# Optimization experiments

Measured on AMD Instinct MI355X. Metric: run time of the kernel, lower is better.

## Reference

```python
import jax, jax.numpy as jnp
import numpy as np
from math import ceil

CAPACITY_FACTOR = 2.0
MIN_CAPACITY = 4


def setup_inputs() -> dict:
    key = jax.random.key(0)
    ks = jax.random.split(key, 4)
    B, S, D, Di, E = 4, 2048, 1024, 4096, 8
    x = jax.random.normal(ks[0], (B, S, D), dtype=jnp.float32)
    Wr = jax.random.normal(ks[1], (D, E), dtype=jnp.float32) * (D ** -0.5)
    W1 = jax.random.normal(ks[2], (E, D, Di), dtype=jnp.float32) * (D ** -0.5)
    b1 = jnp.zeros((E, Di), dtype=jnp.float32)
    W2 = jax.random.normal(ks[3], (E, Di, D), dtype=jnp.float32) * (Di ** -0.5)
    b2 = jnp.zeros((E, D), dtype=jnp.float32)
    return {"x": x, "Wr": Wr, "W1": W1, "b1": b1, "W2": W2, "b2": b2}


def reference(x, Wr, W1, b1, W2, b2):
    B, S, D = x.shape
    E = Wr.shape[1]
    N = B * S
    k = max(MIN_CAPACITY, ceil(N * CAPACITY_FACTOR / E))  # expert capacity (static)

    xt = x.reshape(N, D)
    scores = jax.nn.softmax(xt @ Wr, axis=-1)          # [N, E] router probs
    G, idx = jax.lax.top_k(scores.T, k)                 # [E, k]: each expert picks top-k tokens

    # dispatch: equivalent to P @ x with P = one_hot(idx, N)
    X_in = xt[idx]                                      # [E, k, D]

    # per-expert MLP (batched over experts): Linear -> GELU(exact) -> Linear
    h = jax.nn.gelu(jnp.einsum('ekd,edh->ekh', X_in, W1) + b1[:, None, :], approximate=False)
    X_e = jnp.einsum('ekh,ehd->ekd', h, W2) + b2[:, None, :]  # [E, k, D]

    # combine: einsum('ijl,ij,ijd->ld', P, G, X_e) == scatter-add of G*X_e at idx
    contrib = (G[..., None] * X_e).reshape(E * k, D)
    out = jnp.zeros((N, D), dtype=x.dtype).at[idx.reshape(-1)].add(contrib)
    return out.reshape(B, S, D)
```

## Files before the change

### kernel.cpp

```cpp
#include <hip/hip_runtime.h>
#include <hip/hip_bf16.h>
#include <cstdint>
#include <cstddef>

#define NTOK 8192
#define DMODEL 1024
#define DFF 4096
#define NEXP 8
#define CAP 2048

typedef __attribute__((ext_vector_type(8))) __bf16 bf16x8;
typedef __attribute__((ext_vector_type(4))) float f32x4;

__device__ __forceinline__ void gload16(const void* g, void* l) {
  __builtin_amdgcn_global_load_lds(
      (__attribute__((address_space(1))) void*)(g),
      (__attribute__((address_space(3))) void*)(l),
      16, 0, 0);
}
#define VMWAIT_(n) asm volatile("s_waitcnt vmcnt(" #n ")" ::: "memory")
#define VMWAIT(n) VMWAIT_(n)
#define MEMFENCE asm volatile("" ::: "memory")

__global__ __launch_bounds__(256) void zero_f32(float* p, int n4) {
  int i = blockIdx.x * blockDim.x + threadIdx.x;
  int stride = gridDim.x * blockDim.x;
  float4 z = make_float4(0.f, 0.f, 0.f, 0.f);
  for (; i < n4; i += stride) ((float4*)p)[i] = z;
}

__global__ __launch_bounds__(256) void router_kernel(
    const float* __restrict__ x, const float* __restrict__ Wr,
    float* __restrict__ scoresT, __hip_bfloat16* __restrict__ xb) {
  const int lane = threadIdx.x & 63;
  const int t = blockIdx.x * 4 + (threadIdx.x >> 6);
  const float* xr = x + (size_t)t * DMODEL;
  float acc[NEXP];
#pragma unroll
  for (int j = 0; j < NEXP; ++j) acc[j] = 0.f;
#pragma unroll
  for (int it = 0; it < DMODEL / 64; ++it) {
    int d = it * 64 + lane;
    float xv = xr[d];
    xb[(size_t)t * DMODEL + d] = __float2bfloat16(xv);
    const float4* w = (const float4*)(Wr + (size_t)d * NEXP);
    float4 w0 = w[0], w1 = w[1];
    acc[0] += xv * w0.x; acc[1] += xv * w0.y; acc[2] += xv * w0.z; acc[3] += xv * w0.w;
    acc[4] += xv * w1.x; acc[5] += xv * w1.y; acc[6] += xv * w1.z; acc[7] += xv * w1.w;
  }
#pragma unroll
  for (int off = 32; off; off >>= 1) {
#pragma unroll
    for (int j = 0; j < NEXP; ++j) acc[j] += __shfl_xor(acc[j], off);
  }
  float m = acc[0];
#pragma unroll
  for (int j = 1; j < NEXP; ++j) m = fmaxf(m, acc[j]);
  float s = 0.f;
#pragma unroll
  for (int j = 0; j < NEXP; ++j) { acc[j] = expf(acc[j] - m); s += acc[j]; }
  float inv = 1.f / s;
  if (lane < NEXP) scoresT[(size_t)lane * NTOK + t] = acc[lane] * inv;
}

__global__ __launch_bounds__(256) void topk_kernel(
    const float* __restrict__ scoresT, float* __restrict__ G, int* __restrict__ IDX) {
  __shared__ uint32_t sb[NTOK];
  __shared__ uint32_t hist[256];
  __shared__ uint32_t s_prefix, s_rem;
  __shared__ uint32_t eq_list[256];
  __shared__ uint32_t eq_cnt, gt_cnt;
  const int e = blockIdx.x, tid = threadIdx.x;
  const float* se = scoresT + (size_t)e * NTOK;
  for (int i = tid; i < NTOK; i += 256) sb[i] = __float_as_uint(se[i]);
  if (tid == 0) { s_prefix = 0u; s_rem = CAP; eq_cnt = 0u; gt_cnt = 0u; }
  __syncthreads();
  for (int r = 0; r < 4; ++r) {
    const int shift = 24 - 8 * r;
    for (int i = tid; i < 256; i += 256) hist[i] = 0u;
    __syncthreads();
    uint32_t pfx = s_prefix;
    for (int i = tid; i < NTOK; i += 256) {
      uint32_t b = sb[i];
      if (((b >> shift) >> 8) == pfx) atomicAdd(&hist[(b >> shift) & 255u], 1u);
    }
    __syncthreads();
    if (tid == 0) {
      uint32_t rem = s_rem, cum = 0u;
      int d = 255;
      for (; d > 0; --d) {
        if (cum + hist[d] >= rem) break;
        cum += hist[d];
      }
      s_prefix = (pfx << 8) | (uint32_t)d;
      s_rem = rem - cum;
    }
    __syncthreads();
  }
  const uint32_t T = s_prefix, need = s_rem;
  for (int i = tid; i < NTOK; i += 256) {
    uint32_t b = sb[i];
    if (b > T) {
      uint32_t p = atomicAdd(&gt_cnt, 1u);
      IDX[(size_t)e * CAP + p] = i;
      G[(size_t)e * CAP + p] = __uint_as_float(b);
    } else if (b == T) {
      uint32_t c = atomicAdd(&eq_cnt, 1u);
      if (c < 256u) eq_list[c] = (uint32_t)i;
    }
  }
  __syncthreads();
  if (tid == 0) {
    uint32_t base = gt_cnt;
    uint32_t c = eq_cnt < 256u ? eq_cnt : 256u;
    for (uint32_t s = 0; s < need; ++s) {
      uint32_t mv = 0xFFFFFFFFu; int mi = 0;
      for (uint32_t j = 0; j < c; ++j)
        if (eq_list[j] < mv) { mv = eq_list[j]; mi = (int)j; }
      eq_list[mi] = 0xFFFFFFFFu;
      IDX[(size_t)e * CAP + base + s] = (int)mv;
      G[(size_t)e * CAP + base + s] = __uint_as_float(T);
    }
  }
}

__global__ __launch_bounds__(256) void transpose_cvt(
    const float* __restrict__ in, __hip_bfloat16* __restrict__ out, int R, int C) {
  __shared__ float tile[32][33];
  const int e = blockIdx.z;
  const float* ine = in + (size_t)e * R * C;
  __hip_bfloat16* oute = out + (size_t)e * R * C;
  const int c0 = blockIdx.x * 32, r0 = blockIdx.y * 32;
  const int tx = threadIdx.x, ty = threadIdx.y;
#pragma unroll
  for (int i = 0; i < 4; ++i)
    tile[ty + i * 8][tx] = ine[(size_t)(r0 + ty + i * 8) * C + (c0 + tx)];
  __syncthreads();
#pragma unroll
  for (int i = 0; i < 4; ++i)
    oute[(size_t)(c0 + ty + i * 8) * R + (r0 + tx)] =
        __float2bfloat16(tile[tx][ty + i * 8]);
}


template <int NKT>
__device__ __forceinline__ void gemm_core_v5(
    const char* pa0, const char* pa1, const char* pa2, const char* pa3,
    const char* pb0, const char* pb1, const char* pb2, const char* pb3,
    char* smem, f32x4 (&acc)[8][4]) {
  const int tid = threadIdx.x;
  const int wave = tid >> 6, lane = tid & 63;
  const int wm = wave >> 2, wn = wave & 3;
  const int lrow = lane & 15, lgrp = lane >> 4;
  const int dst = tid * 16;

  const char* pa[4] = {pa0, pa1, pa2, pa3};
  const char* pb[4] = {pb0, pb1, pb2, pb3};

  int offA[8][2], offB[4][2];
#pragma unroll
  for (int mi = 0; mi < 8; ++mi) {
    int rL = wm * 128 + mi * 16 + lrow;
#pragma unroll
    for (int ks = 0; ks < 2; ++ks)
      offA[mi][ks] = rL * 128 + (((ks * 4 + lgrp) + rL & 7) << 4);
  }
#pragma unroll
  for (int mi = 0; mi < 8; ++mi)
#pragma unroll
    for (int ks = 0; ks < 2; ++ks) {
      int rL = wm * 128 + mi * 16 + lrow;
      offA[mi][ks] = rL * 128 + ((((ks * 4 + lgrp) + rL) & 7) << 4);
    }
#pragma unroll
  for (int ni = 0; ni < 4; ++ni) {
    int rL = wn * 64 + ni * 16 + lrow;
#pragma unroll
    for (int ks = 0; ks < 2; ++ks)
      offB[ni][ks] = 32768 + rL * 128 + ((((ks * 4 + lgrp) + rL) & 7) << 4);
  }

#pragma unroll
  for (int g = 0; g < 4; ++g) { gload16(pa[g], smem + g * 8192 + dst); pa[g] += 128; }
#pragma unroll
  for (int g = 0; g < 4; ++g) { gload16(pb[g], smem + 32768 + g * 8192 + dst); pb[g] += 128; }
#pragma unroll
  for (int g = 0; g < 4; ++g) { gload16(pa[g], smem + 65536 + g * 8192 + dst); pa[g] += 128; }
#pragma unroll
  for (int g = 0; g < 4; ++g) { gload16(pb[g], smem + 65536 + 32768 + g * 8192 + dst); pb[g] += 128; }

  for (int kt = 0; kt < NKT; ++kt) {
    char* buf = smem + ((kt & 1) << 16);
    if (kt < NKT - 1) { VMWAIT(8); } else { VMWAIT(0); }
    __builtin_amdgcn_s_barrier();
    MEMFENCE;

    bf16x8 av[8], bv[4];
#pragma unroll
    for (int mi = 0; mi < 8; ++mi) av[mi] = *(const bf16x8*)(buf + offA[mi][0]);
#pragma unroll
    for (int ni = 0; ni < 4; ++ni) bv[ni] = *(const bf16x8*)(buf + offB[ni][0]);

    __builtin_amdgcn_s_setprio(1);
#pragma unroll
    for (int mi = 0; mi < 8; ++mi)
#pragma unroll
      for (int ni = 0; ni < 4; ++ni)
        acc[mi][ni] = __builtin_amdgcn_mfma_f32_16x16x32_bf16(
            av[mi], bv[ni], acc[mi][ni], 0, 0, 0);
    __builtin_amdgcn_s_setprio(0);

    bf16x8 av2[8], bv2[4];
#pragma unroll
    for (int mi = 0; mi < 8; ++mi) av2[mi] = *(const bf16x8*)(buf + offA[mi][1]);
#pragma unroll
    for (int ni = 0; ni < 4; ++ni) bv2[ni] = *(const bf16x8*)(buf + offB[ni][1]);

    asm volatile("s_waitcnt lgkmcnt(0)" ::: "memory");
    __builtin_amdgcn_s_barrier();
    MEMFENCE;
    if (kt < NKT - 2) {
#pragma unroll
      for (int g = 0; g < 4; ++g) { gload16(pa[g], buf + g * 8192 + dst); pa[g] += 128; }
#pragma unroll
      for (int g = 0; g < 4; ++g) { gload16(pb[g], buf + 32768 + g * 8192 + dst); pb[g] += 128; }
    }
    __builtin_amdgcn_sched_barrier(0);
    __builtin_amdgcn_s_setprio(1);
#pragma unroll
    for (int mi = 0; mi < 8; ++mi)
#pragma unroll
      for (int ni = 0; ni < 4; ++ni)
        acc[mi][ni] = __builtin_amdgcn_mfma_f32_16x16x32_bf16(
            av2[mi], bv2[ni], acc[mi][ni], 0, 0, 0);
    __builtin_amdgcn_s_setprio(0);
  }
}

__device__ __forceinline__ float gelu_tanh(float v) {
  float t = 0.7978845608028654f * (v + 0.044715f * v * v * v);
  float e = __expf(2.f * t);
  float th = 1.f - 2.f / (e + 1.f);
  return 0.5f * v * (1.f + th);
}

__global__ __launch_bounds__(512, 2) void gemm1_kernel(
    const __hip_bfloat16* __restrict__ xb,
    const __hip_bfloat16* __restrict__ W1t,
    const float* __restrict__ b1,
    const int* __restrict__ IDX,
    __hip_bfloat16* __restrict__ h, int e0, int nblk) {
  __shared__ __align__(16) char smem[131072];
  int lin = blockIdx.x;
  { int q = nblk >> 3; lin = (lin & 7) * q + (lin >> 3); }
  const int tm = lin & 7, tn = (lin >> 3) & 15, ez = lin >> 7;
  const int e = e0 + ez;
  const int tid = threadIdx.x, wave = tid >> 6, lane = tid & 63;
  const int wm = wave >> 2, wn = wave & 3;
  const int lrow = lane & 15, lgrp = lane >> 4;

  const int r0 = tid >> 3;
  const int ksrc = (((tid & 7) - r0) & 7) * 16;
  const char* pa[4]; const char* pb[4];
#pragma unroll
  for (int g = 0; g < 4; ++g) {
    int m = g * 64 + r0;
    int tok = IDX[e * CAP + tm * 256 + m];
    pa[g] = (const char*)(xb + (size_t)tok * DMODEL) + ksrc;
    int n = g * 64 + r0;
    pb[g] = (const char*)(W1t + ((size_t)e * DFF + tn * 256 + n) * DMODEL) + ksrc;
  }

  f32x4 acc[8][4];
  f32x4 zero = {0.f, 0.f, 0.f, 0.f};
#pragma unroll
  for (int mi = 0; mi < 8; ++mi)
#pragma unroll
    for (int ni = 0; ni < 4; ++ni) acc[mi][ni] = zero;

  gemm_core_v5<DMODEL / 64>(pa[0], pa[1], pa[2], pa[3],
                            pb[0], pb[1], pb[2], pb[3], smem, acc);

  __hip_bfloat16* he = h + (size_t)ez * CAP * DFF;
  const float* b1e = b1 + (size_t)e * DFF;
  float bvals[4];
#pragma unroll
  for (int ni = 0; ni < 4; ++ni)
    bvals[ni] = b1e[tn * 256 + wn * 64 + ni * 16 + lrow];
#pragma unroll
  for (int mi = 0; mi < 8; ++mi) {
#pragma unroll
    for (int j = 0; j < 4; ++j) {
      int row = tm * 256 + wm * 128 + mi * 16 + lgrp * 4 + j;
      __hip_bfloat16* hrow = he + (size_t)row * DFF;
#pragma unroll
      for (int ni = 0; ni < 4; ++ni) {
        int col = tn * 256 + wn * 64 + ni * 16 + lrow;
        float v = acc[mi][ni][j] + bvals[ni];
        hrow[col] = __float2bfloat16(gelu_tanh(v));
      }
    }
  }
}

__global__ __launch_bounds__(512, 2) void gemm2_kernel(
    const __hip_bfloat16* __restrict__ h,
    const __hip_bfloat16* __restrict__ W2t,
    const float* __restrict__ b2,
    const int* __restrict__ IDX, const float* __restrict__ G,
    float* __restrict__ out, int e0, int nblk) {
  __shared__ __align__(16) char smem[131072];
  int lin = blockIdx.x;
  { int q = nblk >> 3; lin = (lin & 7) * q + (lin >> 3); }
  const int tm = lin & 7, tn = (lin >> 3) & 3, ez = lin >> 5;
  const int e = e0 + ez;
  const int tid = threadIdx.x, wave = tid >> 6, lane = tid & 63;
  const int wm = wave >> 2, wn = wave & 3;
  const int lrow = lane & 15, lgrp = lane >> 4;

  const int r0 = tid >> 3;
  const int ksrc = (((tid & 7) - r0) & 7) * 16;
  const char* pa[4]; const char* pb[4];
#pragma unroll
  for (int g = 0; g < 4; ++g) {
    int m = g * 64 + r0;
    pa[g] = (const char*)(h + ((size_t)ez * CAP + tm * 256 + m) * DFF) + ksrc;
    int n = g * 64 + r0;
    pb[g] = (const char*)(W2t + ((size_t)e * DMODEL + tn * 256 + n) * DFF) + ksrc;
  }

  f32x4 acc[8][4];
  f32x4 zero = {0.f, 0.f, 0.f, 0.f};
#pragma unroll
  for (int mi = 0; mi < 8; ++mi)
#pragma unroll
    for (int ni = 0; ni < 4; ++ni) acc[mi][ni] = zero;

  gemm_core_v5<DFF / 64>(pa[0], pa[1], pa[2], pa[3],
                         pb[0], pb[1], pb[2], pb[3], smem, acc);

  const float* b2e = b2 + (size_t)e * DMODEL;
  const int* idxe = IDX + (size_t)e * CAP;
  const float* ge = G + (size_t)e * CAP;
  float bvals[4];
#pragma unroll
  for (int ni = 0; ni < 4; ++ni)
    bvals[ni] = b2e[tn * 256 + wn * 64 + ni * 16 + lrow];
#pragma unroll
  for (int mi = 0; mi < 8; ++mi) {
#pragma unroll
    for (int j = 0; j < 4; ++j) {
      int row = tm * 256 + wm * 128 + mi * 16 + lgrp * 4 + j;
      float g = ge[row];
      int tok = idxe[row];
      float* orow = out + (size_t)tok * DMODEL;
#pragma unroll
      for (int ni = 0; ni < 4; ++ni) {
        int col = tn * 256 + wn * 64 + ni * 16 + lrow;
        atomicAdd(orow + col, (acc[mi][ni][j] + bvals[ni]) * g);
      }
    }
  }
}

extern "C" void kernel_launch(void* const* d_in, const int* in_sizes, int n_in,
                              void* d_out, int out_size, void* d_ws, size_t ws_size,
                              hipStream_t stream) {
  const float* x  = (const float*)d_in[0];
  const float* Wr = (const float*)d_in[1];
  const float* W1 = (const float*)d_in[2];
  const float* b1 = (const float*)d_in[3];
  const float* W2 = (const float*)d_in[4];
  const float* b2 = (const float*)d_in[5];
  float* out = (float*)d_out;
  char* ws = (char*)d_ws;

  size_t off = 0;
  float* scoresT = (float*)(ws + off); off += (size_t)NEXP * NTOK * 4;
  float* G       = (float*)(ws + off); off += (size_t)NEXP * CAP * 4;
  int*   IDX     = (int*)(ws + off);   off += (size_t)NEXP * CAP * 4;
  __hip_bfloat16* xb  = (__hip_bfloat16*)(ws + off); off += (size_t)NTOK * DMODEL * 2;
  __hip_bfloat16* W1t = (__hip_bfloat16*)(ws + off); off += (size_t)NEXP * DFF * DMODEL * 2;
  __hip_bfloat16* W2t = (__hip_bfloat16*)(ws + off); off += (size_t)NEXP * DMODEL * DFF * 2;
  __hip_bfloat16* hbuf = (__hip_bfloat16*)(ws + off);
  size_t h_per_e = (size_t)CAP * DFF * 2;
  size_t avail = (ws_size > off) ? (ws_size - off) : 0;
  int EC = (int)(avail / h_per_e);
  if (EC < 1) EC = 1;
  if (EC > NEXP) EC = NEXP;

  zero_f32<<<512, 256, 0, stream>>>(out, out_size / 4);
  router_kernel<<<NTOK / 4, 256, 0, stream>>>(x, Wr, scoresT, xb);
  topk_kernel<<<NEXP, 256, 0, stream>>>(scoresT, G, IDX);
  transpose_cvt<<<dim3(DFF / 32, DMODEL / 32, NEXP), dim3(32, 8), 0, stream>>>(
      W1, W1t, DMODEL, DFF);
  transpose_cvt<<<dim3(DMODEL / 32, DFF / 32, NEXP), dim3(32, 8), 0, stream>>>(
      W2, W2t, DFF, DMODEL);
  for (int e0 = 0; e0 < NEXP; e0 += EC) {
    int ne = (NEXP - e0 < EC) ? (NEXP - e0) : EC;
    int nblk1 = 128 * ne;
    gemm1_kernel<<<nblk1, 512, 0, stream>>>(xb, W1t, b1, IDX, hbuf, e0, nblk1);
    int nblk2 = 32 * ne;
    gemm2_kernel<<<nblk2, 512, 0, stream>>>(hbuf, W2t, b2, IDX, G, out, e0, nblk2);
  }
}
```

Measured before the change: 475.7 us.

## Replace GEMM core with 8-phase ping-pong schedule interleaving loads and MFMA

Rewrites the shared bf16 GEMM main loop into a four-quadrant, eight-phase schedule per pair of K-tiles. Each phase does a small set of LDS reads and global-to-LDS stages, then an MFMA quadrant bracketed by barriers and priority changes. The goal is finer overlap of global loads, LDS reads and matrix math, in the style of HipKittens-like ping-pong scheduling. It also remaps the smem layout into half-tiles per wave group. In exchange it adds many more barriers per K step and the risk of subtle wait-count or buffer-reuse mistakes.

```diff
diff --git a/kernel.cpp b/kernel.cpp
--- a/kernel.cpp
+++ b/kernel.cpp
@@ -143,8 +143,54 @@
 }
 
 
+#define RD_A(BASE, H)                                                          \
+  {                                                                            \
+    _Pragma("unroll") for (int mi = 0; mi < 4; ++mi)                           \
+        _Pragma("unroll") for (int ks = 0; ks < 2; ++ks) av[mi][ks] =          \
+        *(const bf16x8*)((BASE) + Ab + offA[(H)*4 + mi][ks]);                  \
+  }
+#define RD_B(BASE, BV, H2)                                                     \
+  {                                                                            \
+    _Pragma("unroll") for (int ni = 0; ni < 2; ++ni)                           \
+        _Pragma("unroll") for (int ks = 0; ks < 2; ++ks) BV[ni][ks] =          \
+        *(const bf16x8*)((BASE) + Bb + offB[(H2)*2 + ni][ks]);                 \
+  }
+#define STAGE_A(H, BUF)                                                        \
+  {                                                                            \
+    gload16(pa[(H)*2], (BUF) + (H)*16384 + dst);                               \
+    pa[(H)*2] += 128;                                                          \
+    gload16(pa[(H)*2 + 1], (BUF) + (H)*16384 + 8192 + dst);                    \
+    pa[(H)*2 + 1] += 128;                                                      \
+  }
+#define STAGE_B(H, BUF)                                                        \
+  {                                                                            \
+    gload16(pb[(H)*2], (BUF) + 32768 + (H)*16384 + dst);                       \
+    pb[(H)*2] += 128;                                                          \
+    gload16(pb[(H)*2 + 1], (BUF) + 32768 + (H)*16384 + 8192 + dst);            \
+    pb[(H)*2 + 1] += 128;                                                      \
+  }
+#define PH_PRE                                                                 \
+  __builtin_amdgcn_s_barrier();                                                \
+  MEMFENCE;                                                                    \
+  asm volatile("s_waitcnt lgkmcnt(0)" ::: "memory");                           \
+  __builtin_amdgcn_sched_barrier(0);                                           \
+  __builtin_amdgcn_s_setprio(1);
+#define PH_POST                                                                \
+  __builtin_amdgcn_s_setprio(0);                                               \
+  __builtin_amdgcn_s_barrier();                                                \
+  MEMFENCE;
+#define MFMA_Q(MB, NB, BV)                                                     \
+  {                                                                            \
+    _Pragma("unroll") for (int mi = 0; mi < 4; ++mi)                           \
+        _Pragma("unroll") for (int ni = 0; ni < 2; ++ni)                       \
+            _Pragma("unroll") for (int ks = 0; ks < 2; ++ks)                   \
+                acc[(MB) + mi][(NB) + ni] =                                    \
+        __builtin_amdgcn_mfma_f32_16x16x32_bf16(                               \
+            av[mi][ks], BV[ni][ks], acc[(MB) + mi][(NB) + ni], 0, 0, 0);       \
+  }
+
 template <int NKT>
-__device__ __forceinline__ void gemm_core_v5(
+__device__ __forceinline__ void gemm_core8(
     const char* pa0, const char* pa1, const char* pa2, const char* pa3,
     const char* pb0, const char* pb1, const char* pb2, const char* pb3,
     char* smem, f32x4 (&acc)[8][4]) {
@@ -160,80 +206,80 @@
   int offA[8][2], offB[4][2];
 #pragma unroll
   for (int mi = 0; mi < 8; ++mi) {
-    int rL = wm * 128 + mi * 16 + lrow;
+    int rL = mi * 16 + lrow;
 #pragma unroll
     for (int ks = 0; ks < 2; ++ks)
-      offA[mi][ks] = rL * 128 + (((ks * 4 + lgrp) + rL & 7) << 4);
-  }
-#pragma unroll
-  for (int mi = 0; mi < 8; ++mi)
-#pragma unroll
-    for (int ks = 0; ks < 2; ++ks) {
-      int rL = wm * 128 + mi * 16 + lrow;
       offA[mi][ks] = rL * 128 + ((((ks * 4 + lgrp) + rL) & 7) << 4);
-    }
+  }
 #pragma unroll
   for (int ni = 0; ni < 4; ++ni) {
-    int rL = wn * 64 + ni * 16 + lrow;
+    int rL = (wn & 1) * 64 + ni * 16 + lrow;
 #pragma unroll
     for (int ks = 0; ks < 2; ++ks)
-      offB[ni][ks] = 32768 + rL * 128 + ((((ks * 4 + lgrp) + rL) & 7) << 4);
-  }
-
-#pragma unroll
-  for (int g = 0; g < 4; ++g) { gload16(pa[g], smem + g * 8192 + dst); pa[g] += 128; }
-#pragma unroll
-  for (int g = 0; g < 4; ++g) { gload16(pb[g], smem + 32768 + g * 8192 + dst); pb[g] += 128; }
-#pragma unroll
-  for (int g = 0; g < 4; ++g) { gload16(pa[g], smem + 65536 + g * 8192 + dst); pa[g] += 128; }
-#pragma unroll
-  for (int g = 0; g < 4; ++g) { gload16(pb[g], smem + 65536 + 32768 + g * 8192 + dst); pb[g] += 128; }
-
-  for (int kt = 0; kt < NKT; ++kt) {
-    char* buf = smem + ((kt & 1) << 16);
-    if (kt < NKT - 1) { VMWAIT(8); } else { VMWAIT(0); }
+      offB[ni][ks] = rL * 128 + ((((ks * 4 + lgrp) + rL) & 7) << 4);
+  }
+  const int Ab = wm * 16384;
+  const int Bb = 32768 + (wn >> 1) * 16384;
+
+  char* b0 = smem;
+  char* b1 = smem + 65536;
+
+#pragma unroll
+  for (int g = 0; g < 4; ++g) {
+    gload16(pa[g], b0 + (g >> 1) * 16384 + (g & 1) * 8192 + dst);
+    pa[g] += 128;
+  }
+#pragma unroll
+  for (int g = 0; g < 4; ++g) {
+    gload16(pb[g], b0 + 32768 + (g >> 1) * 16384 + (g & 1) * 8192 + dst);
+    pb[g] += 128;
+  }
+#pragma unroll
+  for (int g = 0; g < 4; ++g) {
+    gload16(pb[g], b1 + 32768 + (g >> 1) * 16384 + (g & 1) * 8192 + dst);
+    pb[g] += 128;
+  }
+  VMWAIT(4);
+  __builtin_amdgcn_s_barrier();
+  MEMFENCE;
+
+  bf16x8 av[4][2], bv0[2][2], bv1[2][2];
+
+  for (int i = 0; i < NKT / 2; ++i) {
+    const bool st2 = (2 * i + 2 < NKT);
+    const bool st3 = (2 * i + 3 < NKT);
+
+    RD_A(b0, 0); RD_B(b0, bv0, 0);
+    STAGE_A(0, b1);
+    PH_PRE; MFMA_Q(0, 0, bv0); PH_POST;
+    RD_B(b0, bv1, 1);
+    STAGE_A(1, b1);
+    PH_PRE; MFMA_Q(0, 2, bv1); PH_POST;
+    RD_A(b0, 1);
+    if (st2) STAGE_B(0, b0);
+    PH_PRE; MFMA_Q(4, 2, bv1); PH_POST;
+    if (st2) STAGE_B(1, b0);
+    PH_PRE; MFMA_Q(4, 0, bv0);
+    __builtin_amdgcn_s_setprio(0);
+    if (st2) { VMWAIT(4); } else { VMWAIT(0); }
     __builtin_amdgcn_s_barrier();
     MEMFENCE;
 
-    bf16x8 av[8], bv[4];
-#pragma unroll
-    for (int mi = 0; mi < 8; ++mi) av[mi] = *(const bf16x8*)(buf + offA[mi][0]);
-#pragma unroll
-    for (int ni = 0; ni < 4; ++ni) bv[ni] = *(const bf16x8*)(buf + offB[ni][0]);
-
-    __builtin_amdgcn_s_setprio(1);
-#pragma unroll
-    for (int mi = 0; mi < 8; ++mi)
-#pragma unroll
-      for (int ni = 0; ni < 4; ++ni)
-        acc[mi][ni] = __builtin_amdgcn_mfma_f32_16x16x32_bf16(
-            av[mi], bv[ni], acc[mi][ni], 0, 0, 0);
+    RD_A(b1, 0); RD_B(b1, bv0, 0);
+    if (st2) STAGE_A(0, b0);
+    PH_PRE; MFMA_Q(0, 0, bv0); PH_POST;
+    RD_B(b1, bv1, 1);
+    if (st2) STAGE_A(1, b0);
+    PH_PRE; MFMA_Q(0, 2, bv1); PH_POST;
+    RD_A(b1, 1);
+    if (st3) STAGE_B(0, b1);
+    PH_PRE; MFMA_Q(4, 2, bv1); PH_POST;
+    if (st3) STAGE_B(1, b1);
+    PH_PRE; MFMA_Q(4, 0, bv0);
     __builtin_amdgcn_s_setprio(0);
-
-    bf16x8 av2[8], bv2[4];
-#pragma unroll
-    for (int mi = 0; mi < 8; ++mi) av2[mi] = *(const bf16x8*)(buf + offA[mi][1]);
-#pragma unroll
-    for (int ni = 0; ni < 4; ++ni) bv2[ni] = *(const bf16x8*)(buf + offB[ni][1]);
-
-    asm volatile("s_waitcnt lgkmcnt(0)" ::: "memory");
+    if (st3) { VMWAIT(4); }
     __builtin_amdgcn_s_barrier();
     MEMFENCE;
-    if (kt < NKT - 2) {
-#pragma unroll
-      for (int g = 0; g < 4; ++g) { gload16(pa[g], buf + g * 8192 + dst); pa[g] += 128; }
-#pragma unroll
-      for (int g = 0; g < 4; ++g) { gload16(pb[g], buf + 32768 + g * 8192 + dst); pb[g] += 128; }
-    }
-    __builtin_amdgcn_sched_barrier(0);
-    __builtin_amdgcn_s_setprio(1);
-#pragma unroll
-    for (int mi = 0; mi < 8; ++mi)
-#pragma unroll
-      for (int ni = 0; ni < 4; ++ni)
-        acc[mi][ni] = __builtin_amdgcn_mfma_f32_16x16x32_bf16(
-            av2[mi], bv2[ni], acc[mi][ni], 0, 0, 0);
-    __builtin_amdgcn_s_setprio(0);
   }
 }
 
@@ -278,8 +324,8 @@
 #pragma unroll
     for (int ni = 0; ni < 4; ++ni) acc[mi][ni] = zero;
 
-  gemm_core_v5<DMODEL / 64>(pa[0], pa[1], pa[2], pa[3],
-                            pb[0], pb[1], pb[2], pb[3], smem, acc);
+  gemm_core8<DMODEL / 64>(pa[0], pa[1], pa[2], pa[3],
+                          pb[0], pb[1], pb[2], pb[3], smem, acc);
 
   __hip_bfloat16* he = h + (size_t)ez * CAP * DFF;
   const float* b1e = b1 + (size_t)e * DFF;
@@ -336,8 +382,8 @@
 #pragma unroll
     for (int ni = 0; ni < 4; ++ni) acc[mi][ni] = zero;
 
-  gemm_core_v5<DFF / 64>(pa[0], pa[1], pa[2], pa[3],
-                         pb[0], pb[1], pb[2], pb[3], smem, acc);
+  gemm_core8<DFF / 64>(pa[0], pa[1], pa[2], pa[3],
+                       pb[0], pb[1], pb[2], pb[3], smem, acc);
 
   const float* b2e = b2 + (size_t)e * DMODEL;
   const int* idxe = IDX + (size_t)e * CAP;
```

Result: no change. 472.2 us (-0.7%).
